# Optimization experiments

Hardware: AMD Instinct MI355X
Metric: run time of the kernel (lower is better)

Reference implementation:

```python
import jax, jax.numpy as jnp
import numpy as np

LOSS_WEIGHT = 1.0
INTENSITY_WEIGHT = 0.5


def setup_inputs() -> dict:
    key = jax.random.key(0)
    k1, k2 = jax.random.split(key)
    N, M = 20000, 20000
    adv_pc = jax.random.normal(k1, (N, 4), dtype=jnp.float32)
    ori_pc = jax.random.normal(k2, (M, 4), dtype=jnp.float32)
    return {"adv_pc": adv_pc, "ori_pc": ori_pc}


def reference(adv_pc, ori_pc):
    adv_xyz = adv_pc[:, :3]  # [N,3]
    ori_xyz = ori_pc[:, :3]  # [M,3]

    # Squared pairwise distances via |a|^2 + |b|^2 - 2 a.b  -> [N,M]
    a2 = jnp.sum(adv_xyz * adv_xyz, axis=1)  # [N]
    b2 = jnp.sum(ori_xyz * ori_xyz, axis=1)  # [M]
    d2 = a2[:, None] + b2[None, :] - 2.0 * (adv_xyz @ ori_xyz.T)

    # 1-NN in both directions (knn_points with K=1 returns squared dists)
    min_dist_adv_to_ori = jnp.min(d2, axis=1)     # [N]
    adv_indices = jnp.argmin(d2, axis=1)          # [N] nearest ori for each adv
    min_dist_ori_to_adv = jnp.min(d2, axis=0)     # [M]
    ori_indices = jnp.argmin(d2, axis=0)          # [M] nearest adv for each ori

    chamfer_loss = jnp.mean(min_dist_adv_to_ori) + jnp.mean(min_dist_ori_to_adv)

    adv_intensity = adv_pc[:, 3]
    ori_intensity = ori_pc[:, 3]
    adv_intensity_diff_1 = jnp.mean((adv_intensity - ori_intensity[adv_indices]) ** 2)
    adv_intensity_diff_2 = jnp.mean((ori_intensity - adv_intensity[ori_indices]) ** 2)
    intensity_loss = (adv_intensity_diff_1 + adv_intensity_diff_2) / 2.0

    return chamfer_loss * LOSS_WEIGHT + intensity_loss * INTENSITY_WEIGHT
```

## Files before the change

kernel.cpp:

```cpp
#include <hip/hip_runtime.h>

#define CH 512
#define TPCH 16
#define QPB 128
#define YSL 8
#define RB 64

typedef __bf16 bf16x8 __attribute__((ext_vector_type(8)));
typedef float f32x16 __attribute__((ext_vector_type(16)));

__device__ __forceinline__ unsigned bfb(float x) {
    __bf16 h = (__bf16)x;
    return (unsigned)__builtin_bit_cast(unsigned short, h);
}
__device__ __forceinline__ float bff(unsigned b) {
    return (float)__builtin_bit_cast(__bf16, (unsigned short)b);
}

__device__ __forceinline__ void stage_one(uint4* a_lds, int local, float4 p, bool valid) {
    float x, y, z, u;
    if (valid) {
        x = p.x; y = p.y; z = p.z;
        u = 0.25f * fmaf(p.x, p.x, fmaf(p.y, p.y, p.z * p.z));
    } else {
        x = 0.f; y = 0.f; z = 0.f; u = 130.f;
    }
    unsigned xh = bfb(x); unsigned xl = bfb(x - bff(xh));
    unsigned yh = bfb(y); unsigned yl = bfb(y - bff(yh));
    unsigned zh = bfb(z); unsigned zl = bfb(z - bff(zh));
    unsigned uh = bfb(u); float u1 = u - bff(uh);
    unsigned ul = bfb(u1); unsigned ull = bfb(u1 - bff(ul));
    uint4 h0, h1;
    h0.x = xh | (xl << 16); h0.y = h0.x;
    h0.z = yh | (yl << 16); h0.w = h0.z;
    h1.x = zh | (zl << 16); h1.y = h1.x;
    h1.z = uh | (ul << 16);
    h1.w = ull | (0x43A0u << 16);
    int t = local >> 5, r = local & 31;
    a_lds[t * 64 + r]      = h0;
    a_lds[t * 64 + 32 + r] = h1;
}

__global__ __launch_bounds__(256, 6) void mfma_nn(
    const float4* __restrict__ adv, int N,
    const float4* __restrict__ ori, int M,
    unsigned long long* __restrict__ slots, int S,
    int chunks)
{
    const int dir = blockIdx.z;
    const float4* __restrict__ q = dir ? ori : adv;
    const float4* __restrict__ t = dir ? adv : ori;
    const int nq = dir ? M : N;
    const int nt = dir ? N : M;
    unsigned long long* __restrict__ outrow =
        slots + (size_t)(dir * YSL + blockIdx.y) * (size_t)S;

    const int tid = threadIdx.x;
    const int wave = tid >> 6;
    const int lane = tid & 63;
    const int col = lane & 31;
    const int h = lane >> 5;

    const int qi = blockIdx.x * QPB + wave * 32 + col;
    const bool qv = qi < nq;
    float4 qp = qv ? q[qi] : make_float4(0.f, 0.f, 0.f, 0.f);

    float cx = -0.5f * qp.x, cy = -0.5f * qp.y, cz = -0.5f * qp.z;
    unsigned cxh = bfb(cx); unsigned cxl = bfb(cx - bff(cxh));
    unsigned cyh = bfb(cy); unsigned cyl = bfb(cy - bff(cyh));
    unsigned czh = bfb(cz); unsigned czl = bfb(cz - bff(czh));
    uint4 braw;
    if (h == 0) {
        braw.x = cxh | (cxh << 16); braw.y = cxl | (cxl << 16);
        braw.z = cyh | (cyh << 16); braw.w = cyl | (cyl << 16);
    } else {
        braw.x = czh | (czh << 16); braw.y = czl | (czl << 16);
        braw.z = 0x3F803F80u;       braw.w = 0x3F803F80u;
    }
    const bf16x8 bfrag = __builtin_bit_cast(bf16x8, braw);

    __shared__ uint4 a_lds[TPCH * 64];
    const f32x16 zero = {};

    const int slicebase = blockIdx.y * chunks * CH;
    unsigned cm = 0xFFFFFFFFu;
    int base = slicebase;

    float4 pf0, pf1; bool v0, v1;
    {
        int j0 = base + tid, j1 = j0 + 256;
        if (base + CH <= nt) {
            pf0 = t[j0]; pf1 = t[j1]; v0 = true; v1 = true;
        } else {
            v0 = j0 < nt; v1 = j1 < nt;
            pf0 = v0 ? t[j0] : make_float4(0.f, 0.f, 0.f, 0.f);
            pf1 = v1 ? t[j1] : make_float4(0.f, 0.f, 0.f, 0.f);
        }
    }

    for (int c = 0; c < chunks; ++c) {
        if (c) __syncthreads();
        stage_one(a_lds, tid,       pf0, v0);
        stage_one(a_lds, tid + 256, pf1, v1);
        __syncthreads();

        const int nb = base + CH;
        if (c + 1 < chunks) {
            int j0 = nb + tid, j1 = j0 + 256;
            if (nb + CH <= nt) {
                pf0 = t[j0]; pf1 = t[j1]; v0 = true; v1 = true;
            } else {
                v0 = j0 < nt; v1 = j1 < nt;
                pf0 = v0 ? t[j0] : make_float4(0.f, 0.f, 0.f, 0.f);
                pf1 = v1 ? t[j1] : make_float4(0.f, 0.f, 0.f, 0.f);
            }
        }

        const unsigned tl0 = (unsigned)(c << 4);
        #pragma unroll
        for (int tt = 0; tt < TPCH; ++tt) {
            bf16x8 a = __builtin_bit_cast(bf16x8, a_lds[tt * 64 + lane]);
            f32x16 acc = __builtin_amdgcn_mfma_f32_32x32x16_bf16(a, bfrag, zero, 0, 0, 0);

            unsigned u0 = min(min(__float_as_uint(acc[0]),  __float_as_uint(acc[1])),  __float_as_uint(acc[2]));
            unsigned u1 = min(min(__float_as_uint(acc[3]),  __float_as_uint(acc[4])),  __float_as_uint(acc[5]));
            unsigned u2 = min(min(__float_as_uint(acc[6]),  __float_as_uint(acc[7])),  __float_as_uint(acc[8]));
            unsigned u3 = min(min(__float_as_uint(acc[9]),  __float_as_uint(acc[10])), __float_as_uint(acc[11]));
            unsigned u4 = min(min(__float_as_uint(acc[12]), __float_as_uint(acc[13])), __float_as_uint(acc[14]));
            unsigned u5 = min(min(u0, u1), u2);
            unsigned u6 = min(min(u3, u4), __float_as_uint(acc[15]));
            unsigned m  = min(u5, u6);

            cm = min(cm, (m << 9) | (tl0 + (unsigned)tt));
        }
        base = nb;
    }

    const int jb = slicebase + (int)(cm & 0x7Fu) * 32 + 4 * h;
    unsigned long long run = 0xFFFFFFFFFFFFFFFFull;
    #pragma unroll
    for (int e = 0; e < 16; ++e) {
        int r = (e & 3) + ((e >> 2) << 3);
        int j = jb + r;
        if (j < nt) {
            float4 b = t[j];
            float dx = qp.x - b.x, dy = qp.y - b.y, dz = qp.z - b.z;
            float d2 = fmaf(dx, dx, fmaf(dy, dy, dz * dz));
            unsigned long long cand =
                ((unsigned long long)__float_as_uint(d2) << 32) | (unsigned)j;
            run = cand < run ? cand : run;
        }
    }

    unsigned long long other = __shfl_xor(run, 32);
    run = run < other ? run : other;
    if (h == 0 && qv) outrow[qi] = run;
}

__device__ inline float block_reduce_sum(float v, float* lds) {
    #pragma unroll
    for (int off = 32; off > 0; off >>= 1) v += __shfl_down(v, off, 64);
    int wave = threadIdx.x >> 6;
    int lane = threadIdx.x & 63;
    __syncthreads();
    if (lane == 0) lds[wave] = v;
    __syncthreads();
    float r = 0.f;
    if (threadIdx.x == 0) {
        #pragma unroll
        for (int w = 0; w < 4; ++w) r += lds[w];
    }
    return r;
}

__global__ __launch_bounds__(256) void partial_finalize(
    const unsigned long long* __restrict__ slots, int S,
    int n, int m,
    const float4* __restrict__ adv, const float4* __restrict__ ori,
    float* __restrict__ partials)
{
    __shared__ float lds[4];
    float s_min0 = 0.f, s_i1 = 0.f, s_min1 = 0.f, s_i2 = 0.f;
    const int stride = RB * 256;
    const int t0 = blockIdx.x * 256 + threadIdx.x;
    const unsigned long long* __restrict__ s0 = slots;
    const unsigned long long* __restrict__ s1 = slots + (size_t)YSL * S;

    for (int i = t0; i < n; i += stride) {
        unsigned long long k = s0[i];
        #pragma unroll
        for (int y = 1; y < YSL; ++y) k = min(k, s0[(size_t)y * S + i]);
        int j = (int)(unsigned int)(k & 0xFFFFFFFFu);
        s_min0 += __uint_as_float((unsigned int)(k >> 32));
        float dw = adv[i].w - ori[j].w;
        s_i1 += dw * dw;
    }
    for (int jj = t0; jj < m; jj += stride) {
        unsigned long long k = s1[jj];
        #pragma unroll
        for (int y = 1; y < YSL; ++y) k = min(k, s1[(size_t)y * S + jj]);
        int i = (int)(unsigned int)(k & 0xFFFFFFFFu);
        s_min1 += __uint_as_float((unsigned int)(k >> 32));
        float dw = ori[jj].w - adv[i].w;
        s_i2 += dw * dw;
    }

    float r0 = block_reduce_sum(s_min0, lds);
    float r1 = block_reduce_sum(s_i1, lds);
    float r2 = block_reduce_sum(s_min1, lds);
    float r3 = block_reduce_sum(s_i2, lds);

    if (threadIdx.x == 0) {
        partials[blockIdx.x * 4 + 0] = r0;
        partials[blockIdx.x * 4 + 1] = r1;
        partials[blockIdx.x * 4 + 2] = r2;
        partials[blockIdx.x * 4 + 3] = r3;
    }
}

__global__ __launch_bounds__(256) void combine(
    const float* __restrict__ partials, int n, int m, float* __restrict__ out)
{
    __shared__ float lds[4];
    float v0 = 0.f, v1 = 0.f, v2 = 0.f, v3 = 0.f;
    if (threadIdx.x < RB) {
        v0 = partials[threadIdx.x * 4 + 0];
        v1 = partials[threadIdx.x * 4 + 1];
        v2 = partials[threadIdx.x * 4 + 2];
        v3 = partials[threadIdx.x * 4 + 3];
    }
    float r0 = block_reduce_sum(v0, lds);
    float r1 = block_reduce_sum(v1, lds);
    float r2 = block_reduce_sum(v2, lds);
    float r3 = block_reduce_sum(v3, lds);
    if (threadIdx.x == 0) {
        float chamfer   = r0 / (float)n + r2 / (float)m;
        float intensity = 0.5f * (r1 / (float)n + r3 / (float)m);
        out[0] = chamfer * 1.0f + intensity * 0.5f;
    }
}

extern "C" void kernel_launch(void* const* d_in, const int* in_sizes, int n_in,
                              void* d_out, int out_size, void* d_ws, size_t ws_size,
                              hipStream_t stream) {
    const float4* adv = (const float4*)d_in[0];
    const float4* ori = (const float4*)d_in[1];
    const int N = in_sizes[0] / 4;
    const int M = in_sizes[1] / 4;
    const int S = max(N, M);

    unsigned long long* slots = (unsigned long long*)d_ws;
    float* partials = (float*)(slots + (size_t)2 * YSL * S);
    float* out = (float*)d_out;

    const int chunks = (S + YSL * CH - 1) / (YSL * CH);
    dim3 grid((S + QPB - 1) / QPB, YSL, 2);
    mfma_nn<<<grid, 256, 0, stream>>>(adv, N, ori, M, slots, S, chunks);

    partial_finalize<<<RB, 256, 0, stream>>>(slots, S, N, M, adv, ori, partials);
    combine<<<1, 256, 0, stream>>>(partials, N, M, out);
}
```

Before: 49.33 us.

## Drop register prefetch of target chunk and raise occupancy bound to 8 waves

```diff
diff --git a/kernel.cpp b/kernel.cpp
--- a/kernel.cpp
+++ b/kernel.cpp
@@ -41,7 +41,7 @@
     a_lds[t * 64 + 32 + r] = h1;
 }
 
-__global__ __launch_bounds__(256, 6) void mfma_nn(
+__global__ __launch_bounds__(256, 8) void mfma_nn(
     const float4* __restrict__ adv, int N,
     const float4* __restrict__ ori, int M,
     unsigned long long* __restrict__ slots, int S,
@@ -80,47 +80,34 @@
     const bf16x8 bfrag = __builtin_bit_cast(bf16x8, braw);
 
     __shared__ uint4 a_lds[TPCH * 64];
-    const f32x16 zero = {};
 
     const int slicebase = blockIdx.y * chunks * CH;
     unsigned cm = 0xFFFFFFFFu;
     int base = slicebase;
 
-    float4 pf0, pf1; bool v0, v1;
-    {
-        int j0 = base + tid, j1 = j0 + 256;
-        if (base + CH <= nt) {
-            pf0 = t[j0]; pf1 = t[j1]; v0 = true; v1 = true;
-        } else {
-            v0 = j0 < nt; v1 = j1 < nt;
-            pf0 = v0 ? t[j0] : make_float4(0.f, 0.f, 0.f, 0.f);
-            pf1 = v1 ? t[j1] : make_float4(0.f, 0.f, 0.f, 0.f);
-        }
-    }
-
     for (int c = 0; c < chunks; ++c) {
         if (c) __syncthreads();
-        stage_one(a_lds, tid,       pf0, v0);
-        stage_one(a_lds, tid + 256, pf1, v1);
-        __syncthreads();
-
-        const int nb = base + CH;
-        if (c + 1 < chunks) {
-            int j0 = nb + tid, j1 = j0 + 256;
-            if (nb + CH <= nt) {
-                pf0 = t[j0]; pf1 = t[j1]; v0 = true; v1 = true;
+        {
+            int j0 = base + tid, j1 = j0 + 256;
+            if (base + CH <= nt) {
+                stage_one(a_lds, tid,       t[j0], true);
+                stage_one(a_lds, tid + 256, t[j1], true);
             } else {
-                v0 = j0 < nt; v1 = j1 < nt;
-                pf0 = v0 ? t[j0] : make_float4(0.f, 0.f, 0.f, 0.f);
-                pf1 = v1 ? t[j1] : make_float4(0.f, 0.f, 0.f, 0.f);
+                bool v0 = j0 < nt, v1 = j1 < nt;
+                float4 p0 = v0 ? t[j0] : make_float4(0.f, 0.f, 0.f, 0.f);
+                float4 p1 = v1 ? t[j1] : make_float4(0.f, 0.f, 0.f, 0.f);
+                stage_one(a_lds, tid,       p0, v0);
+                stage_one(a_lds, tid + 256, p1, v1);
             }
         }
+        __syncthreads();
 
         const unsigned tl0 = (unsigned)(c << 4);
         #pragma unroll
         for (int tt = 0; tt < TPCH; ++tt) {
             bf16x8 a = __builtin_bit_cast(bf16x8, a_lds[tt * 64 + lane]);
-            f32x16 acc = __builtin_amdgcn_mfma_f32_32x32x16_bf16(a, bfrag, zero, 0, 0, 0);
+            f32x16 acc = {};
+            acc = __builtin_amdgcn_mfma_f32_32x32x16_bf16(a, bfrag, acc, 0, 0, 0);
 
             unsigned u0 = min(min(__float_as_uint(acc[0]),  __float_as_uint(acc[1])),  __float_as_uint(acc[2]));
             unsigned u1 = min(min(__float_as_uint(acc[3]),  __float_as_uint(acc[4])),  __float_as_uint(acc[5]));
@@ -133,7 +120,7 @@
 
             cm = min(cm, (m << 9) | (tl0 + (unsigned)tt));
         }
-        base = nb;
+        base += CH;
     }
 
     const int jb = slicebase + (int)(cm & 0x7Fu) * 32 + 4 * h;
```

After: 49.11 us. Within noise of the previous version (-0.4%).
